# Performance work log

Measured on AMD Instinct MI355X. Metric: run time of the kernel, lower is better.

Reference implementation:

```python
import jax, jax.numpy as jnp
import numpy as np

NUM_HEADS = 16
BLOCK_SIZE = 64


def setup_inputs() -> dict:
    key = jax.random.key(0)
    ks = jax.random.split(key, 5)
    B, S, C = 2, 2047, 1024
    return {
        "x": jax.random.normal(ks[0], (B, S, C), dtype=jnp.float32),
        "global_token": jax.random.normal(ks[1], (1, 1, C), dtype=jnp.float32),
        "qkv_w": jax.random.normal(ks[2], (3 * C, C), dtype=jnp.float32) * 0.02,
        "proj_w": jax.random.normal(ks[3], (C, C), dtype=jnp.float32) * 0.02,
        "proj_b": jax.random.normal(ks[4], (C,), dtype=jnp.float32) * 0.02,
    }


def reference(x, global_token, qkv_w, proj_w, proj_b):
    B, S, C = x.shape
    H = NUM_HEADS
    D = C // H
    scale = D ** -0.5
    # prepend global token -> N = S + 1
    g = jnp.broadcast_to(global_token, (B, 1, C))
    xg = jnp.concatenate([g, x], axis=1)
    N = S + 1
    # fused qkv projection (torch Linear: x @ W^T)
    qkv = (xg @ qkv_w.T).reshape(B, N, 3, H, D)
    qkv = jnp.transpose(qkv, (2, 0, 3, 1, 4))  # [3, B, H, N, D]
    q, k, v = qkv[0], qkv[1], qkv[2]
    # block-causal mask: query t sees key j iff block(j) <= block(t)
    blk = jnp.arange(N) // BLOCK_SIZE
    mask = blk[:, None] >= blk[None, :]  # [N, N]
    attn = jnp.einsum("bhqd,bhkd->bhqk", q, k) * scale
    attn = jnp.where(mask[None, None], attn, -jnp.inf)
    attn = jax.nn.softmax(attn, axis=-1)
    out = jnp.einsum("bhqk,bhkd->bhqd", attn, v)
    out = jnp.transpose(out, (0, 2, 1, 3)).reshape(B, N, C)
    out = out[:, 1:, :]  # drop global token
    return out @ proj_w.T + proj_b
```

## Files before the change

kernel.cpp:

```cpp
#include <hip/hip_runtime.h>
#include <math.h>

typedef _Float16 h16;
typedef _Float16 half8 __attribute__((ext_vector_type(8)));
typedef float f32x4 __attribute__((ext_vector_type(4)));

#define NB 2
#define NS 2047
#define NC 1024
#define NN 2048
#define NH 16
#define ND 64

__device__ __forceinline__ void gl_lds16(const h16* g, h16* l) {
  __builtin_amdgcn_global_load_lds((const __attribute__((address_space(1))) void*)g,
                                   (__attribute__((address_space(3))) void*)l, 16, 0, 0);
}
__device__ __forceinline__ f32x4 mfma16(half8 a, half8 b, f32x4 c) {
  return __builtin_amdgcn_mfma_f32_16x16x32_f16(a, b, c, 0, 0, 0);
}

__global__ __launch_bounds__(256) void cast_xg_k(
    const float* __restrict__ x, const float* __restrict__ g, h16* __restrict__ out) {
  size_t i = ((size_t)blockIdx.x * 256 + threadIdx.x) * 16;
  const int c = (int)(i & (NC - 1));
  const int n = (int)((i >> 10) & (NN - 1));
  const int b = (int)(i >> 21);
  const float* src = (n == 0) ? (g + c) : (x + ((size_t)b * NS + (n - 1)) * NC + c);
  h16 tmp[16];
#pragma unroll
  for (int j = 0; j < 4; ++j) {
    float4 f = ((const float4*)src)[j];
    tmp[4 * j + 0] = (h16)f.x; tmp[4 * j + 1] = (h16)f.y;
    tmp[4 * j + 2] = (h16)f.z; tmp[4 * j + 3] = (h16)f.w;
  }
  *(half8*)(out + i) = *(half8*)&tmp[0];
  *(half8*)(out + i + 8) = *(half8*)&tmp[8];
}

__global__ __launch_bounds__(256) void cast_f16_k(
    const float* __restrict__ in, h16* __restrict__ out) {
  size_t i = ((size_t)blockIdx.x * 256 + threadIdx.x) * 8;
  float4 f0 = ((const float4*)(in + i))[0];
  float4 f1 = ((const float4*)(in + i))[1];
  h16 tmp[8];
  tmp[0] = (h16)f0.x; tmp[1] = (h16)f0.y; tmp[2] = (h16)f0.z; tmp[3] = (h16)f0.w;
  tmp[4] = (h16)f1.x; tmp[5] = (h16)f1.y; tmp[6] = (h16)f1.z; tmp[7] = (h16)f1.w;
  *(half8*)(out + i) = *(half8*)&tmp[0];
}

__global__ __launch_bounds__(256) void gemm_qkv_h(
    const h16* __restrict__ A, const h16* __restrict__ W, h16* __restrict__ out) {
  __shared__ h16 As[128 * 32];
  __shared__ h16 Bs[128 * 32];
  const int tid = threadIdx.x;
  const int m0 = blockIdx.y * 128, j0 = blockIdx.x * 128;
  const int wid = tid >> 6, lane = tid & 63, l15 = lane & 15, quad = lane >> 4;
  const h16* ag = A + (size_t)(m0 + wid * 32 + (lane >> 2)) * NC + (lane & 3) * 8;
  const h16* bg = W + (size_t)(j0 + wid * 32 + (lane >> 2)) * NC + (lane & 3) * 8;
  h16* lA = &As[wid * 32 * 32];
  h16* lB = &Bs[wid * 32 * 32];
  f32x4 acc[2][8];
#pragma unroll
  for (int rt = 0; rt < 2; ++rt)
#pragma unroll
    for (int ct = 0; ct < 8; ++ct) acc[rt][ct] = (f32x4){0.f, 0.f, 0.f, 0.f};

  for (int k0 = 0; k0 < NC; k0 += 32) {
    __syncthreads();
    gl_lds16(ag + k0, lA);
    gl_lds16(ag + k0 + 16 * NC, lA + 16 * 32);
    gl_lds16(bg + k0, lB);
    gl_lds16(bg + k0 + 16 * NC, lB + 16 * 32);
    __syncthreads();
    half8 af0 = *(const half8*)&As[(wid * 32 + l15) * 32 + quad * 8];
    half8 af1 = *(const half8*)&As[(wid * 32 + 16 + l15) * 32 + quad * 8];
#pragma unroll
    for (int ct = 0; ct < 8; ++ct) {
      half8 bf = *(const half8*)&Bs[(ct * 16 + l15) * 32 + quad * 8];
      acc[0][ct] = mfma16(af0, bf, acc[0][ct]);
      acc[1][ct] = mfma16(af1, bf, acc[1][ct]);
    }
  }
#pragma unroll
  for (int rt = 0; rt < 2; ++rt)
#pragma unroll
    for (int ct = 0; ct < 8; ++ct)
#pragma unroll
      for (int r = 0; r < 4; ++r) {
        const int mm = m0 + wid * 32 + rt * 16 + quad * 4 + r;
        const int jj = j0 + ct * 16 + l15;
        out[(size_t)mm * (3 * NC) + jj] = (h16)acc[rt][ct][r];
      }
}

__global__ __launch_bounds__(256) void vtrans_k(
    const h16* __restrict__ qkvh, h16* __restrict__ vT) {
  __shared__ h16 ts[64 * 72];
  const int kb = blockIdx.x, h = blockIdx.y, b = blockIdx.z;
  const int t = threadIdx.x;
  const int key = t >> 2, co = (t & 3) * 16;
  const h16* src = qkvh + (size_t)(b * NN + kb * 64 + key) * (3 * NC) + 2 * NC + h * ND + co;
  half8 v0 = *(const half8*)src;
  half8 v1 = *(const half8*)(src + 8);
  *(half8*)&ts[key * 72 + co] = v0;
  *(half8*)&ts[key * 72 + co + 8] = v1;
  __syncthreads();
  const int d = t >> 2, ko = (t & 3) * 16;
  h16 buf[16];
#pragma unroll
  for (int i = 0; i < 16; ++i) buf[i] = ts[(ko + i) * 72 + d];
  h16* dst = vT + ((size_t)(b * NH + h) * ND + d) * NN + kb * 64 + ko;
  *(half8*)dst = *(half8*)&buf[0];
  *(half8*)(dst + 8) = *(half8*)&buf[8];
}

__device__ __forceinline__ void attn_tile(
    half8 aq0, half8 aq1, const h16* Ks, const h16* Vs, h16* Pw,
    int l15, int quad, f32x4* o, float* den) {
  f32x4 s[4];
#pragma unroll
  for (int ct = 0; ct < 4; ++ct) {
    half8 bk0 = *(const half8*)&Ks[(ct * 16 + l15) * 72 + quad * 8];
    half8 bk1 = *(const half8*)&Ks[(ct * 16 + l15) * 72 + 32 + quad * 8];
    f32x4 z = (f32x4){0.f, 0.f, 0.f, 0.f};
    z = mfma16(aq0, bk0, z);
    s[ct] = mfma16(aq1, bk1, z);
  }
#pragma unroll
  for (int ct = 0; ct < 4; ++ct)
#pragma unroll
    for (int r = 0; r < 4; ++r) {
      float p = __expf(s[ct][r] * 0.125f);
      den[r] += p;
      Pw[(quad * 4 + r) * 72 + ct * 16 + l15] = (h16)p;
    }
  half8 ap0 = *(const half8*)&Pw[l15 * 72 + quad * 8];
  half8 ap1 = *(const half8*)&Pw[l15 * 72 + 32 + quad * 8];
#pragma unroll
  for (int ct = 0; ct < 4; ++ct) {
    half8 bv0 = *(const half8*)&Vs[(ct * 16 + l15) * 72 + quad * 8];
    half8 bv1 = *(const half8*)&Vs[(ct * 16 + l15) * 72 + 32 + quad * 8];
    o[ct] = mfma16(ap0, bv0, o[ct]);
    o[ct] = mfma16(ap1, bv1, o[ct]);
  }
}

__global__ __launch_bounds__(256) void attn_h(
    const h16* __restrict__ qkvh, const h16* __restrict__ vT, h16* __restrict__ outp) {
  __shared__ h16 Ks[64 * 72];
  __shared__ h16 Vs[64 * 72];
  __shared__ h16 Ps[128 * 72];
  const int q1 = blockIdx.x;
  const int q2 = 31 - q1;
  const int h = blockIdx.y, b = blockIdx.z;
  const int tid = threadIdx.x, wid = tid >> 6, lane = tid & 63;
  const int l15 = lane & 15, quad = lane >> 4;
  const h16* q1src = qkvh + (size_t)(b * NN + q1 * 64 + wid * 16 + l15) * (3 * NC) + h * ND + quad * 8;
  const h16* q2src = qkvh + (size_t)(b * NN + q2 * 64 + wid * 16 + l15) * (3 * NC) + h * ND + quad * 8;
  half8 a1q0 = *(const half8*)q1src;
  half8 a1q1 = *(const half8*)(q1src + 32);
  half8 a2q0 = *(const half8*)q2src;
  half8 a2q1 = *(const half8*)(q2src + 32);
  f32x4 o1[4], o2[4];
  float d1[4] = {0.f, 0.f, 0.f, 0.f}, d2[4] = {0.f, 0.f, 0.f, 0.f};
#pragma unroll
  for (int ct = 0; ct < 4; ++ct) {
    o1[ct] = (f32x4){0.f, 0.f, 0.f, 0.f};
    o2[ct] = (f32x4){0.f, 0.f, 0.f, 0.f};
  }
  const int skey = tid >> 2, sco = (tid & 3) * 16;
  const h16* kbase = qkvh + (size_t)(b * NN + skey) * (3 * NC) + NC + h * ND + sco;
  const h16* vbase = vT + ((size_t)(b * NH + h) * ND + skey) * NN + sco;
  h16* P1 = &Ps[(wid * 16) * 72];
  h16* P2 = &Ps[(64 + wid * 16) * 72];

  for (int kb = 0; kb <= q2; ++kb) {
    const h16* kp = kbase + (size_t)kb * 64 * (3 * NC);
    half8 k0 = *(const half8*)kp;
    half8 k1 = *(const half8*)(kp + 8);
    const h16* vp = vbase + kb * 64;
    half8 v0 = *(const half8*)vp;
    half8 v1 = *(const half8*)(vp + 8);
    __syncthreads();
    *(half8*)&Ks[skey * 72 + sco] = k0; *(half8*)&Ks[skey * 72 + sco + 8] = k1;
    *(half8*)&Vs[skey * 72 + sco] = v0; *(half8*)&Vs[skey * 72 + sco + 8] = v1;
    __syncthreads();
    attn_tile(a2q0, a2q1, Ks, Vs, P2, l15, quad, o2, d2);
    if (kb <= q1) attn_tile(a1q0, a1q1, Ks, Vs, P1, l15, quad, o1, d1);
  }
#pragma unroll
  for (int r = 0; r < 4; ++r)
#pragma unroll
    for (int off = 1; off < 16; off <<= 1) {
      d1[r] += __shfl_xor(d1[r], off);
      d2[r] += __shfl_xor(d2[r], off);
    }
#pragma unroll
  for (int ct = 0; ct < 4; ++ct)
#pragma unroll
    for (int r = 0; r < 4; ++r) {
      const int n1 = q1 * 64 + wid * 16 + quad * 4 + r;
      const int n2 = q2 * 64 + wid * 16 + quad * 4 + r;
      outp[(size_t)(b * NN + n1) * NC + h * ND + ct * 16 + l15] = (h16)(o1[ct][r] / d1[r]);
      outp[(size_t)(b * NN + n2) * NC + h * ND + ct * 16 + l15] = (h16)(o2[ct][r] / d2[r]);
    }
}

__global__ __launch_bounds__(256) void gemm_proj_h(
    const h16* __restrict__ Ah, const h16* __restrict__ W,
    const float* __restrict__ bias, float* __restrict__ out) {
  __shared__ h16 As[64 * 32];
  __shared__ h16 Bs[128 * 32];
  const int tid = threadIdx.x;
  const int m0 = blockIdx.y * 64, j0 = blockIdx.x * 128;
  const int wid = tid >> 6, lane = tid & 63, l15 = lane & 15, quad = lane >> 4;
  int m = m0 + wid * 16 + (lane >> 2);
  if (m > NB * NS - 1) m = NB * NS - 1;
  const int bb = (m >= NS) ? 1 : 0;
  const h16* ag = Ah + (size_t)(bb * NN + m - bb * NS + 1) * NC + (lane & 3) * 8;
  const h16* bg = W + (size_t)(j0 + wid * 32 + (lane >> 2)) * NC + (lane & 3) * 8;
  h16* lA = &As[wid * 16 * 32];
  h16* lB = &Bs[wid * 32 * 32];
  f32x4 acc[8];
#pragma unroll
  for (int ct = 0; ct < 8; ++ct) acc[ct] = (f32x4){0.f, 0.f, 0.f, 0.f};

  for (int k0 = 0; k0 < NC; k0 += 32) {
    __syncthreads();
    gl_lds16(ag + k0, lA);
    gl_lds16(bg + k0, lB);
    gl_lds16(bg + k0 + 16 * NC, lB + 16 * 32);
    __syncthreads();
    half8 af = *(const half8*)&As[(wid * 16 + l15) * 32 + quad * 8];
#pragma unroll
    for (int ct = 0; ct < 8; ++ct) {
      half8 bf = *(const half8*)&Bs[(ct * 16 + l15) * 32 + quad * 8];
      acc[ct] = mfma16(af, bf, acc[ct]);
    }
  }
#pragma unroll
  for (int ct = 0; ct < 8; ++ct) {
    const float bv = bias[j0 + ct * 16 + l15];
#pragma unroll
    for (int r = 0; r < 4; ++r) {
      const int mm = m0 + wid * 16 + quad * 4 + r;
      if (mm < NB * NS)
        out[(size_t)mm * NC + j0 + ct * 16 + l15] = acc[ct][r] + bv;
    }
  }
}

extern "C" void kernel_launch(void* const* d_in, const int* in_sizes, int n_in,
                              void* d_out, int out_size, void* d_ws, size_t ws_size,
                              hipStream_t stream) {
  const float* x = (const float*)d_in[0];
  const float* g = (const float*)d_in[1];
  const float* qkv_w = (const float*)d_in[2];
  const float* proj_w = (const float*)d_in[3];
  const float* proj_b = (const float*)d_in[4];
  float* out = (float*)d_out;

  h16* xgh  = (h16*)d_ws;
  h16* w3h  = xgh + (size_t)NB * NN * NC;
  h16* wph  = w3h + (size_t)3 * NC * NC;
  h16* qkvh = wph + (size_t)NC * NC;
  h16* vTh  = qkvh + (size_t)NB * NN * 3 * NC;
  h16* attnh = vTh + (size_t)NB * NH * ND * NN;

  cast_xg_k<<<dim3(1024), 256, 0, stream>>>(x, g, xgh);
  cast_f16_k<<<dim3(1536), 256, 0, stream>>>(qkv_w, w3h);
  cast_f16_k<<<dim3(512), 256, 0, stream>>>(proj_w, wph);
  gemm_qkv_h<<<dim3(24, 32), 256, 0, stream>>>(xgh, w3h, qkvh);
  vtrans_k<<<dim3(32, NH, NB), 256, 0, stream>>>(qkvh, vTh);
  attn_h<<<dim3(16, NH, NB), 256, 0, stream>>>(qkvh, vTh, attnh);
  gemm_proj_h<<<dim3(8, 64), 256, 0, stream>>>(attnh, wph, proj_b, out);
}
```

Before: 204.0 us.

## Restructure GEMMs to 2x2 warp tiles, register-stream K/V in attention, merge weight casts

Both GEMMs now use a 2x2 warp layout, load A fragments straight from global memory into registers, and stage only B in LDS in a k-major layout with a 64-wide K step. The attention kernel drops the LDS staging of K and V. Each wave loads its own K/V fragments into registers and prefetches the next K tile, uses a remapped 1D grid, and splits the loop so the short query block is handled without a per-iteration branch. The two weight-cast launches are merged into one. These changes aim to cut LDS traffic, barriers and launch count, at the cost of redundant global loads per wave and higher register pressure.

```diff
diff --git a/kernel.cpp b/kernel.cpp
--- a/kernel.cpp
+++ b/kernel.cpp
@@ -38,58 +38,71 @@
   *(half8*)(out + i + 8) = *(half8*)&tmp[8];
 }
 
-__global__ __launch_bounds__(256) void cast_f16_k(
-    const float* __restrict__ in, h16* __restrict__ out) {
+__global__ __launch_bounds__(256) void cast_w_k(
+    const float* __restrict__ qw, const float* __restrict__ pw, h16* __restrict__ out) {
   size_t i = ((size_t)blockIdx.x * 256 + threadIdx.x) * 8;
-  float4 f0 = ((const float4*)(in + i))[0];
-  float4 f1 = ((const float4*)(in + i))[1];
+  const float* src = (i < (size_t)3 * NC * NC) ? (qw + i) : (pw + (i - (size_t)3 * NC * NC));
+  float4 f0 = ((const float4*)src)[0];
+  float4 f1 = ((const float4*)src)[1];
   h16 tmp[8];
   tmp[0] = (h16)f0.x; tmp[1] = (h16)f0.y; tmp[2] = (h16)f0.z; tmp[3] = (h16)f0.w;
   tmp[4] = (h16)f1.x; tmp[5] = (h16)f1.y; tmp[6] = (h16)f1.z; tmp[7] = (h16)f1.w;
   *(half8*)(out + i) = *(half8*)&tmp[0];
 }
 
-__global__ __launch_bounds__(256) void gemm_qkv_h(
+__global__ __launch_bounds__(256, 3) void gemm_qkv_h(
     const h16* __restrict__ A, const h16* __restrict__ W, h16* __restrict__ out) {
-  __shared__ h16 As[128 * 32];
-  __shared__ h16 Bs[128 * 32];
+  __shared__ h16 Bs[8 * 128 * 8];
   const int tid = threadIdx.x;
   const int m0 = blockIdx.y * 128, j0 = blockIdx.x * 128;
   const int wid = tid >> 6, lane = tid & 63, l15 = lane & 15, quad = lane >> 4;
-  const h16* ag = A + (size_t)(m0 + wid * 32 + (lane >> 2)) * NC + (lane & 3) * 8;
-  const h16* bg = W + (size_t)(j0 + wid * 32 + (lane >> 2)) * NC + (lane & 3) * 8;
-  h16* lA = &As[wid * 32 * 32];
-  h16* lB = &Bs[wid * 32 * 32];
-  f32x4 acc[2][8];
-#pragma unroll
-  for (int rt = 0; rt < 2; ++rt)
-#pragma unroll
-    for (int ct = 0; ct < 8; ++ct) acc[rt][ct] = (f32x4){0.f, 0.f, 0.f, 0.f};
-
-  for (int k0 = 0; k0 < NC; k0 += 32) {
+  const int w0 = wid & 1, w1 = wid >> 1;
+  const h16* abase = A + (size_t)(m0 + w1 * 64 + l15) * NC + quad * 8;
+  const h16* bW = W + (size_t)(j0 + lane) * NC;
+  f32x4 acc[4][4];
+#pragma unroll
+  for (int rt = 0; rt < 4; ++rt)
+#pragma unroll
+    for (int ct = 0; ct < 4; ++ct) acc[rt][ct] = (f32x4){0.f, 0.f, 0.f, 0.f};
+
+  for (int k0 = 0; k0 < NC; k0 += 64) {
     __syncthreads();
-    gl_lds16(ag + k0, lA);
-    gl_lds16(ag + k0 + 16 * NC, lA + 16 * 32);
-    gl_lds16(bg + k0, lB);
-    gl_lds16(bg + k0 + 16 * NC, lB + 16 * 32);
+#pragma unroll
+    for (int s = 0; s < 2; ++s) {
+      const int k8 = wid * 2 + s;
+#pragma unroll
+      for (int jo = 0; jo < 2; ++jo)
+        gl_lds16(bW + (size_t)jo * 64 * NC + k0 + k8 * 8, &Bs[(k8 * 128 + jo * 64) * 8]);
+    }
     __syncthreads();
-    half8 af0 = *(const half8*)&As[(wid * 32 + l15) * 32 + quad * 8];
-    half8 af1 = *(const half8*)&As[(wid * 32 + 16 + l15) * 32 + quad * 8];
-#pragma unroll
-    for (int ct = 0; ct < 8; ++ct) {
-      half8 bf = *(const half8*)&Bs[(ct * 16 + l15) * 32 + quad * 8];
-      acc[0][ct] = mfma16(af0, bf, acc[0][ct]);
-      acc[1][ct] = mfma16(af1, bf, acc[1][ct]);
-    }
-  }
-#pragma unroll
-  for (int rt = 0; rt < 2; ++rt)
-#pragma unroll
-    for (int ct = 0; ct < 8; ++ct)
+    half8 af[4][2];
+#pragma unroll
+    for (int rt = 0; rt < 4; ++rt) {
+      af[rt][0] = *(const half8*)(abase + (size_t)rt * 16 * NC + k0);
+      af[rt][1] = *(const half8*)(abase + (size_t)rt * 16 * NC + k0 + 32);
+    }
+    half8 bf[4][2];
+#pragma unroll
+    for (int ct = 0; ct < 4; ++ct) {
+      bf[ct][0] = *(const half8*)&Bs[((quad)*128 + w0 * 64 + ct * 16 + l15) * 8];
+      bf[ct][1] = *(const half8*)&Bs[((4 + quad) * 128 + w0 * 64 + ct * 16 + l15) * 8];
+    }
+#pragma unroll
+    for (int rt = 0; rt < 4; ++rt)
+#pragma unroll
+      for (int ct = 0; ct < 4; ++ct) {
+        acc[rt][ct] = mfma16(af[rt][0], bf[ct][0], acc[rt][ct]);
+        acc[rt][ct] = mfma16(af[rt][1], bf[ct][1], acc[rt][ct]);
+      }
+  }
+#pragma unroll
+  for (int rt = 0; rt < 4; ++rt)
+#pragma unroll
+    for (int ct = 0; ct < 4; ++ct)
 #pragma unroll
       for (int r = 0; r < 4; ++r) {
-        const int mm = m0 + wid * 32 + rt * 16 + quad * 4 + r;
-        const int jj = j0 + ct * 16 + l15;
+        const int mm = m0 + w1 * 64 + rt * 16 + quad * 4 + r;
+        const int jj = j0 + w0 * 64 + ct * 16 + l15;
         out[(size_t)mm * (3 * NC) + jj] = (h16)acc[rt][ct][r];
       }
 }
@@ -115,53 +128,30 @@
   *(half8*)(dst + 8) = *(half8*)&buf[8];
 }
 
-__device__ __forceinline__ void attn_tile(
-    half8 aq0, half8 aq1, const h16* Ks, const h16* Vs, h16* Pw,
-    int l15, int quad, f32x4* o, float* den) {
-  f32x4 s[4];
-#pragma unroll
-  for (int ct = 0; ct < 4; ++ct) {
-    half8 bk0 = *(const half8*)&Ks[(ct * 16 + l15) * 72 + quad * 8];
-    half8 bk1 = *(const half8*)&Ks[(ct * 16 + l15) * 72 + 32 + quad * 8];
-    f32x4 z = (f32x4){0.f, 0.f, 0.f, 0.f};
-    z = mfma16(aq0, bk0, z);
-    s[ct] = mfma16(aq1, bk1, z);
-  }
-#pragma unroll
-  for (int ct = 0; ct < 4; ++ct)
-#pragma unroll
-    for (int r = 0; r < 4; ++r) {
-      float p = __expf(s[ct][r] * 0.125f);
-      den[r] += p;
-      Pw[(quad * 4 + r) * 72 + ct * 16 + l15] = (h16)p;
-    }
-  half8 ap0 = *(const half8*)&Pw[l15 * 72 + quad * 8];
-  half8 ap1 = *(const half8*)&Pw[l15 * 72 + 32 + quad * 8];
-#pragma unroll
-  for (int ct = 0; ct < 4; ++ct) {
-    half8 bv0 = *(const half8*)&Vs[(ct * 16 + l15) * 72 + quad * 8];
-    half8 bv1 = *(const half8*)&Vs[(ct * 16 + l15) * 72 + 32 + quad * 8];
-    o[ct] = mfma16(ap0, bv0, o[ct]);
-    o[ct] = mfma16(ap1, bv1, o[ct]);
-  }
-}
-
-__global__ __launch_bounds__(256) void attn_h(
+#define PST 68
+__global__ __launch_bounds__(256, 2) void attn_h(
     const h16* __restrict__ qkvh, const h16* __restrict__ vT, h16* __restrict__ outp) {
-  __shared__ h16 Ks[64 * 72];
-  __shared__ h16 Vs[64 * 72];
-  __shared__ h16 Ps[128 * 72];
-  const int q1 = blockIdx.x;
-  const int q2 = 31 - q1;
-  const int h = blockIdx.y, b = blockIdx.z;
+  __shared__ h16 Ps[128 * PST];
+  const int wg = blockIdx.x;
+  const int bh = (wg & 7) * 4 + ((wg >> 3) & 3);
+  const int pr = wg >> 5;
+  const int b = bh >> 4, h = bh & 15;
+  const int q1 = pr, q2 = 31 - pr;
   const int tid = threadIdx.x, wid = tid >> 6, lane = tid & 63;
   const int l15 = lane & 15, quad = lane >> 4;
+  h16* Pw2 = &Ps[(wid * 32) * PST];
+  h16* Pw1 = Pw2 + 16 * PST;
+
   const h16* q1src = qkvh + (size_t)(b * NN + q1 * 64 + wid * 16 + l15) * (3 * NC) + h * ND + quad * 8;
   const h16* q2src = qkvh + (size_t)(b * NN + q2 * 64 + wid * 16 + l15) * (3 * NC) + h * ND + quad * 8;
   half8 a1q0 = *(const half8*)q1src;
   half8 a1q1 = *(const half8*)(q1src + 32);
   half8 a2q0 = *(const half8*)q2src;
   half8 a2q1 = *(const half8*)(q2src + 32);
+
+  const h16* kp0 = qkvh + ((size_t)(b * NN + l15) * 3 + 1) * NC + h * ND + quad * 8;
+  const h16* vp0 = vT + ((size_t)(b * NH + h) * ND + l15) * NN + quad * 8;
+
   f32x4 o1[4], o2[4];
   float d1[4] = {0.f, 0.f, 0.f, 0.f}, d2[4] = {0.f, 0.f, 0.f, 0.f};
 #pragma unroll
@@ -169,26 +159,65 @@
     o1[ct] = (f32x4){0.f, 0.f, 0.f, 0.f};
     o2[ct] = (f32x4){0.f, 0.f, 0.f, 0.f};
   }
-  const int skey = tid >> 2, sco = (tid & 3) * 16;
-  const h16* kbase = qkvh + (size_t)(b * NN + skey) * (3 * NC) + NC + h * ND + sco;
-  const h16* vbase = vT + ((size_t)(b * NH + h) * ND + skey) * NN + sco;
-  h16* P1 = &Ps[(wid * 16) * 72];
-  h16* P2 = &Ps[(64 + wid * 16) * 72];
-
-  for (int kb = 0; kb <= q2; ++kb) {
-    const h16* kp = kbase + (size_t)kb * 64 * (3 * NC);
-    half8 k0 = *(const half8*)kp;
-    half8 k1 = *(const half8*)(kp + 8);
-    const h16* vp = vbase + kb * 64;
-    half8 v0 = *(const half8*)vp;
-    half8 v1 = *(const half8*)(vp + 8);
-    __syncthreads();
-    *(half8*)&Ks[skey * 72 + sco] = k0; *(half8*)&Ks[skey * 72 + sco + 8] = k1;
-    *(half8*)&Vs[skey * 72 + sco] = v0; *(half8*)&Vs[skey * 72 + sco + 8] = v1;
-    __syncthreads();
-    attn_tile(a2q0, a2q1, Ks, Vs, P2, l15, quad, o2, d2);
-    if (kb <= q1) attn_tile(a1q0, a1q1, Ks, Vs, P1, l15, quad, o1, d1);
-  }
+
+#define LOADK(kb, kf)                                                        \
+  {                                                                          \
+    const h16* p_ = kp0 + (size_t)(kb) * 64 * (3 * NC);                      \
+    _Pragma("unroll") for (int ct = 0; ct < 4; ++ct) {                       \
+      kf[2 * ct] = *(const half8*)(p_ + (size_t)ct * 16 * (3 * NC));         \
+      kf[2 * ct + 1] = *(const half8*)(p_ + (size_t)ct * 16 * (3 * NC) + 32);\
+    }                                                                        \
+  }
+#define LOADV(kb, vf)                                                        \
+  {                                                                          \
+    const h16* p_ = vp0 + (kb) * 64;                                         \
+    _Pragma("unroll") for (int ct = 0; ct < 4; ++ct) {                       \
+      vf[2 * ct] = *(const half8*)(p_ + (size_t)ct * 16 * NN);               \
+      vf[2 * ct + 1] = *(const half8*)(p_ + (size_t)ct * 16 * NN + 32);      \
+    }                                                                        \
+  }
+#define TILE(aq0, aq1, kf, vf, Pw, o, den)                                   \
+  {                                                                          \
+    f32x4 s_[4];                                                             \
+    _Pragma("unroll") for (int ct = 0; ct < 4; ++ct) {                       \
+      f32x4 z_ = (f32x4){0.f, 0.f, 0.f, 0.f};                                \
+      z_ = mfma16(aq0, kf[2 * ct], z_);                                      \
+      s_[ct] = mfma16(aq1, kf[2 * ct + 1], z_);                              \
+    }                                                                        \
+    _Pragma("unroll") for (int ct = 0; ct < 4; ++ct)                         \
+        _Pragma("unroll") for (int r = 0; r < 4; ++r) {                      \
+      float p_ = __expf(s_[ct][r] * 0.125f);                                 \
+      den[r] += p_;                                                          \
+      Pw[(quad * 4 + r) * PST + ct * 16 + l15] = (h16)p_;                    \
+    }                                                                        \
+    half8 ap0_ = *(const half8*)&Pw[l15 * PST + quad * 8];                   \
+    half8 ap1_ = *(const half8*)&Pw[l15 * PST + 32 + quad * 8];              \
+    _Pragma("unroll") for (int ct = 0; ct < 4; ++ct) {                       \
+      o[ct] = mfma16(ap0_, vf[2 * ct], o[ct]);                               \
+      o[ct] = mfma16(ap1_, vf[2 * ct + 1], o[ct]);                           \
+    }                                                                        \
+  }
+
+  half8 kf[8], kfn[8], vf[8];
+  LOADK(0, kf);
+  for (int kb = 0; kb <= q1; ++kb) {
+    LOADV(kb, vf);
+    const int nkb = (kb + 1 <= q2) ? kb + 1 : q2;
+    LOADK(nkb, kfn);
+    TILE(a2q0, a2q1, kf, vf, Pw2, o2, d2);
+    TILE(a1q0, a1q1, kf, vf, Pw1, o1, d1);
+#pragma unroll
+    for (int i = 0; i < 8; ++i) kf[i] = kfn[i];
+  }
+  for (int kb = q1 + 1; kb <= q2; ++kb) {
+    LOADV(kb, vf);
+    const int nkb = (kb + 1 <= q2) ? kb + 1 : q2;
+    LOADK(nkb, kfn);
+    TILE(a2q0, a2q1, kf, vf, Pw2, o2, d2);
+#pragma unroll
+    for (int i = 0; i < 8; ++i) kf[i] = kfn[i];
+  }
+
 #pragma unroll
   for (int r = 0; r < 4; ++r)
 #pragma unroll
@@ -207,48 +236,71 @@
     }
 }
 
-__global__ __launch_bounds__(256) void gemm_proj_h(
+__global__ __launch_bounds__(256, 2) void gemm_proj_h(
     const h16* __restrict__ Ah, const h16* __restrict__ W,
     const float* __restrict__ bias, float* __restrict__ out) {
-  __shared__ h16 As[64 * 32];
-  __shared__ h16 Bs[128 * 32];
+  __shared__ h16 Bs[8 * 128 * 8];
   const int tid = threadIdx.x;
   const int m0 = blockIdx.y * 64, j0 = blockIdx.x * 128;
   const int wid = tid >> 6, lane = tid & 63, l15 = lane & 15, quad = lane >> 4;
-  int m = m0 + wid * 16 + (lane >> 2);
-  if (m > NB * NS - 1) m = NB * NS - 1;
-  const int bb = (m >= NS) ? 1 : 0;
-  const h16* ag = Ah + (size_t)(bb * NN + m - bb * NS + 1) * NC + (lane & 3) * 8;
-  const h16* bg = W + (size_t)(j0 + wid * 32 + (lane >> 2)) * NC + (lane & 3) * 8;
-  h16* lA = &As[wid * 16 * 32];
-  h16* lB = &Bs[wid * 32 * 32];
-  f32x4 acc[8];
-#pragma unroll
-  for (int ct = 0; ct < 8; ++ct) acc[ct] = (f32x4){0.f, 0.f, 0.f, 0.f};
-
-  for (int k0 = 0; k0 < NC; k0 += 32) {
+  const int w0 = wid & 1, w1 = wid >> 1;
+  const h16* abase[2];
+#pragma unroll
+  for (int rt = 0; rt < 2; ++rt) {
+    int m = m0 + w1 * 32 + rt * 16 + l15;
+    if (m > NB * NS - 1) m = NB * NS - 1;
+    const int bb = (m >= NS) ? 1 : 0;
+    abase[rt] = Ah + (size_t)(bb * NN + m - bb * NS + 1) * NC + quad * 8;
+  }
+  const h16* bW = W + (size_t)(j0 + lane) * NC;
+  f32x4 acc[2][4];
+#pragma unroll
+  for (int rt = 0; rt < 2; ++rt)
+#pragma unroll
+    for (int ct = 0; ct < 4; ++ct) acc[rt][ct] = (f32x4){0.f, 0.f, 0.f, 0.f};
+
+  for (int k0 = 0; k0 < NC; k0 += 64) {
     __syncthreads();
-    gl_lds16(ag + k0, lA);
-    gl_lds16(bg + k0, lB);
-    gl_lds16(bg + k0 + 16 * NC, lB + 16 * 32);
+#pragma unroll
+    for (int s = 0; s < 2; ++s) {
+      const int k8 = wid * 2 + s;
+#pragma unroll
+      for (int jo = 0; jo < 2; ++jo)
+        gl_lds16(bW + (size_t)jo * 64 * NC + k0 + k8 * 8, &Bs[(k8 * 128 + jo * 64) * 8]);
+    }
     __syncthreads();
-    half8 af = *(const half8*)&As[(wid * 16 + l15) * 32 + quad * 8];
-#pragma unroll
-    for (int ct = 0; ct < 8; ++ct) {
-      half8 bf = *(const half8*)&Bs[(ct * 16 + l15) * 32 + quad * 8];
-      acc[ct] = mfma16(af, bf, acc[ct]);
-    }
-  }
-#pragma unroll
-  for (int ct = 0; ct < 8; ++ct) {
-    const float bv = bias[j0 + ct * 16 + l15];
-#pragma unroll
-    for (int r = 0; r < 4; ++r) {
-      const int mm = m0 + wid * 16 + quad * 4 + r;
-      if (mm < NB * NS)
-        out[(size_t)mm * NC + j0 + ct * 16 + l15] = acc[ct][r] + bv;
-    }
-  }
+    half8 af[2][2];
+#pragma unroll
+    for (int rt = 0; rt < 2; ++rt) {
+      af[rt][0] = *(const half8*)(abase[rt] + k0);
+      af[rt][1] = *(const half8*)(abase[rt] + k0 + 32);
+    }
+    half8 bf[4][2];
+#pragma unroll
+    for (int ct = 0; ct < 4; ++ct) {
+      bf[ct][0] = *(const half8*)&Bs[((quad)*128 + w0 * 64 + ct * 16 + l15) * 8];
+      bf[ct][1] = *(const half8*)&Bs[((4 + quad) * 128 + w0 * 64 + ct * 16 + l15) * 8];
+    }
+#pragma unroll
+    for (int rt = 0; rt < 2; ++rt)
+#pragma unroll
+      for (int ct = 0; ct < 4; ++ct) {
+        acc[rt][ct] = mfma16(af[rt][0], bf[ct][0], acc[rt][ct]);
+        acc[rt][ct] = mfma16(af[rt][1], bf[ct][1], acc[rt][ct]);
+      }
+  }
+#pragma unroll
+  for (int rt = 0; rt < 2; ++rt)
+#pragma unroll
+    for (int ct = 0; ct < 4; ++ct) {
+      const int jj = j0 + w0 * 64 + ct * 16 + l15;
+      const float bv = bias[jj];
+#pragma unroll
+      for (int r = 0; r < 4; ++r) {
+        const int mm = m0 + w1 * 32 + rt * 16 + quad * 4 + r;
+        if (mm < NB * NS) out[(size_t)mm * NC + jj] = acc[rt][ct][r] + bv;
+      }
+    }
 }
 
 extern "C" void kernel_launch(void* const* d_in, const int* in_sizes, int n_in,
@@ -269,10 +321,9 @@
   h16* attnh = vTh + (size_t)NB * NH * ND * NN;
 
   cast_xg_k<<<dim3(1024), 256, 0, stream>>>(x, g, xgh);
-  cast_f16_k<<<dim3(1536), 256, 0, stream>>>(qkv_w, w3h);
-  cast_f16_k<<<dim3(512), 256, 0, stream>>>(proj_w, wph);
+  cast_w_k<<<dim3(2048), 256, 0, stream>>>(qkv_w, proj_w, w3h);
   gemm_qkv_h<<<dim3(24, 32), 256, 0, stream>>>(xgh, w3h, qkvh);
   vtrans_k<<<dim3(32, NH, NB), 256, 0, stream>>>(qkvh, vTh);
-  attn_h<<<dim3(16, NH, NB), 256, 0, stream>>>(qkvh, vTh, attnh);
+  attn_h<<<dim3(512), 256, 0, stream>>>(qkvh, vTh, attnh);
   gemm_proj_h<<<dim3(8, 64), 256, 0, stream>>>(attnh, wph, proj_b, out);
 }
```

After: 299.5 us. 46.8% more time.

## Rewrite attention with per-wave key split and double-buffered async loads; widen GEMM K-tiles

Applied to the files above, without the earlier changes.

Attention now launches one block per query tile, ordered longest first. Each of the four waves handles a disjoint quarter of every key block, loaded asynchronously into double-buffered LDS with waitcnt-based per-wave sync, and the partial outputs and denominators are reduced across waves through LDS at the end. P is kept in registers by feeding it to a 16x16x16 MFMA as the B operand, which removes the LDS round trip for P. Both GEMMs move to 64-wide K tiles with XOR-swizzled LDS, and the two weight casts merge into one launch. This targets LDS traffic, the per-iteration block barriers and launch overhead, at the cost of more LDS use and an extra cross-wave reduction.

```diff
diff --git a/kernel.cpp b/kernel.cpp
--- a/kernel.cpp
+++ b/kernel.cpp
@@ -3,6 +3,7 @@
 
 typedef _Float16 h16;
 typedef _Float16 half8 __attribute__((ext_vector_type(8)));
+typedef _Float16 half4 __attribute__((ext_vector_type(4)));
 typedef float f32x4 __attribute__((ext_vector_type(4)));
 
 #define NB 2
@@ -16,9 +17,14 @@
   __builtin_amdgcn_global_load_lds((const __attribute__((address_space(1))) void*)g,
                                    (__attribute__((address_space(3))) void*)l, 16, 0, 0);
 }
-__device__ __forceinline__ f32x4 mfma16(half8 a, half8 b, f32x4 c) {
+__device__ __forceinline__ f32x4 mfma32(half8 a, half8 b, f32x4 c) {
   return __builtin_amdgcn_mfma_f32_16x16x32_f16(a, b, c, 0, 0, 0);
 }
+__device__ __forceinline__ f32x4 mfma16x(half4 a, half4 b, f32x4 c) {
+  return __builtin_amdgcn_mfma_f32_16x16x16f16(a, b, c, 0, 0, 0);
+}
+#define WAITVM4 __builtin_amdgcn_s_waitcnt(0x0F74)
+#define WAITLG0 __builtin_amdgcn_s_waitcnt(0xC07F)
 
 __global__ __launch_bounds__(256) void cast_xg_k(
     const float* __restrict__ x, const float* __restrict__ g, h16* __restrict__ out) {
@@ -38,11 +44,12 @@
   *(half8*)(out + i + 8) = *(half8*)&tmp[8];
 }
 
-__global__ __launch_bounds__(256) void cast_f16_k(
-    const float* __restrict__ in, h16* __restrict__ out) {
+__global__ __launch_bounds__(256) void cast_w_k(
+    const float* __restrict__ qw, const float* __restrict__ pw, h16* __restrict__ out) {
   size_t i = ((size_t)blockIdx.x * 256 + threadIdx.x) * 8;
-  float4 f0 = ((const float4*)(in + i))[0];
-  float4 f1 = ((const float4*)(in + i))[1];
+  const float* src = (i < (size_t)3 * NC * NC) ? (qw + i) : (pw + (i - (size_t)3 * NC * NC));
+  float4 f0 = ((const float4*)src)[0];
+  float4 f1 = ((const float4*)src)[1];
   h16 tmp[8];
   tmp[0] = (h16)f0.x; tmp[1] = (h16)f0.y; tmp[2] = (h16)f0.z; tmp[3] = (h16)f0.w;
   tmp[4] = (h16)f1.x; tmp[5] = (h16)f1.y; tmp[6] = (h16)f1.z; tmp[7] = (h16)f1.w;
@@ -51,35 +58,39 @@
 
 __global__ __launch_bounds__(256) void gemm_qkv_h(
     const h16* __restrict__ A, const h16* __restrict__ W, h16* __restrict__ out) {
-  __shared__ h16 As[128 * 32];
-  __shared__ h16 Bs[128 * 32];
+  __shared__ h16 As[128 * 64];
+  __shared__ h16 Bs[128 * 64];
   const int tid = threadIdx.x;
   const int m0 = blockIdx.y * 128, j0 = blockIdx.x * 128;
   const int wid = tid >> 6, lane = tid & 63, l15 = lane & 15, quad = lane >> 4;
-  const h16* ag = A + (size_t)(m0 + wid * 32 + (lane >> 2)) * NC + (lane & 3) * 8;
-  const h16* bg = W + (size_t)(j0 + wid * 32 + (lane >> 2)) * NC + (lane & 3) * 8;
-  h16* lA = &As[wid * 32 * 32];
-  h16* lB = &Bs[wid * 32 * 32];
+  const int rl = lane >> 3, cp = lane & 7, csw = cp ^ rl;
+  const h16* ag = A + (size_t)(m0 + wid * 32 + rl) * NC + csw * 8;
+  const h16* bg = W + (size_t)(j0 + wid * 32 + rl) * NC + csw * 8;
   f32x4 acc[2][8];
 #pragma unroll
   for (int rt = 0; rt < 2; ++rt)
 #pragma unroll
     for (int ct = 0; ct < 8; ++ct) acc[rt][ct] = (f32x4){0.f, 0.f, 0.f, 0.f};
 
-  for (int k0 = 0; k0 < NC; k0 += 32) {
-    __syncthreads();
-    gl_lds16(ag + k0, lA);
-    gl_lds16(ag + k0 + 16 * NC, lA + 16 * 32);
-    gl_lds16(bg + k0, lB);
-    gl_lds16(bg + k0 + 16 * NC, lB + 16 * 32);
-    __syncthreads();
-    half8 af0 = *(const half8*)&As[(wid * 32 + l15) * 32 + quad * 8];
-    half8 af1 = *(const half8*)&As[(wid * 32 + 16 + l15) * 32 + quad * 8];
-#pragma unroll
-    for (int ct = 0; ct < 8; ++ct) {
-      half8 bf = *(const half8*)&Bs[(ct * 16 + l15) * 32 + quad * 8];
-      acc[0][ct] = mfma16(af0, bf, acc[0][ct]);
-      acc[1][ct] = mfma16(af1, bf, acc[1][ct]);
+  for (int k0 = 0; k0 < NC; k0 += 64) {
+    __syncthreads();
+#pragma unroll
+    for (int i = 0; i < 4; ++i) {
+      gl_lds16(ag + (size_t)i * 8 * NC + k0, &As[(wid * 32 + i * 8) * 64]);
+      gl_lds16(bg + (size_t)i * 8 * NC + k0, &Bs[(wid * 32 + i * 8) * 64]);
+    }
+    __syncthreads();
+#pragma unroll
+    for (int ks = 0; ks < 2; ++ks) {
+      const int p0 = ((ks * 4 + quad) ^ (l15 & 7)) * 8;
+      half8 af0 = *(const half8*)&As[(wid * 32 + l15) * 64 + p0];
+      half8 af1 = *(const half8*)&As[(wid * 32 + 16 + l15) * 64 + p0];
+#pragma unroll
+      for (int ct = 0; ct < 8; ++ct) {
+        half8 bf = *(const half8*)&Bs[(ct * 16 + l15) * 64 + p0];
+        acc[0][ct] = mfma32(af0, bf, acc[0][ct]);
+        acc[1][ct] = mfma32(af1, bf, acc[1][ct]);
+      }
     }
   }
 #pragma unroll
@@ -115,128 +126,201 @@
   *(half8*)(dst + 8) = *(half8*)&buf[8];
 }
 
-__device__ __forceinline__ void attn_tile(
-    half8 aq0, half8 aq1, const h16* Ks, const h16* Vs, h16* Pw,
-    int l15, int quad, f32x4* o, float* den) {
-  f32x4 s[4];
-#pragma unroll
-  for (int ct = 0; ct < 4; ++ct) {
-    half8 bk0 = *(const half8*)&Ks[(ct * 16 + l15) * 72 + quad * 8];
-    half8 bk1 = *(const half8*)&Ks[(ct * 16 + l15) * 72 + 32 + quad * 8];
-    f32x4 z = (f32x4){0.f, 0.f, 0.f, 0.f};
-    z = mfma16(aq0, bk0, z);
-    s[ct] = mfma16(aq1, bk1, z);
-  }
-#pragma unroll
-  for (int ct = 0; ct < 4; ++ct)
-#pragma unroll
-    for (int r = 0; r < 4; ++r) {
-      float p = __expf(s[ct][r] * 0.125f);
-      den[r] += p;
-      Pw[(quad * 4 + r) * 72 + ct * 16 + l15] = (h16)p;
-    }
-  half8 ap0 = *(const half8*)&Pw[l15 * 72 + quad * 8];
-  half8 ap1 = *(const half8*)&Pw[l15 * 72 + 32 + quad * 8];
-#pragma unroll
-  for (int ct = 0; ct < 4; ++ct) {
-    half8 bv0 = *(const half8*)&Vs[(ct * 16 + l15) * 72 + quad * 8];
-    half8 bv1 = *(const half8*)&Vs[(ct * 16 + l15) * 72 + 32 + quad * 8];
-    o[ct] = mfma16(ap0, bv0, o[ct]);
-    o[ct] = mfma16(ap1, bv1, o[ct]);
-  }
-}
-
-__global__ __launch_bounds__(256) void attn_h(
+__global__ __launch_bounds__(256, 3) void attn_h(
     const h16* __restrict__ qkvh, const h16* __restrict__ vT, h16* __restrict__ outp) {
-  __shared__ h16 Ks[64 * 72];
-  __shared__ h16 Vs[64 * 72];
-  __shared__ h16 Ps[128 * 72];
-  const int q1 = blockIdx.x;
-  const int q2 = 31 - q1;
-  const int h = blockIdx.y, b = blockIdx.z;
-  const int tid = threadIdx.x, wid = tid >> 6, lane = tid & 63;
+  __shared__ h16 K0[4][1024];
+  __shared__ h16 V0[4][1024];
+  __shared__ h16 K1[4][1024];
+  __shared__ h16 V1[4][1024];
+  __shared__ float RED[2 * 64 * 36];
+  __shared__ float DEN[4 * 64];
+  const int bx = blockIdx.x;
+  const int qb = 31 - (bx >> 5);
+  const int bh = bx & 31;
+  const int b = bh >> 4, h = bh & 15;
+  const int tid = threadIdx.x, w = tid >> 6, lane = tid & 63;
   const int l15 = lane & 15, quad = lane >> 4;
-  const h16* q1src = qkvh + (size_t)(b * NN + q1 * 64 + wid * 16 + l15) * (3 * NC) + h * ND + quad * 8;
-  const h16* q2src = qkvh + (size_t)(b * NN + q2 * 64 + wid * 16 + l15) * (3 * NC) + h * ND + quad * 8;
-  half8 a1q0 = *(const half8*)q1src;
-  half8 a1q1 = *(const half8*)(q1src + 32);
-  half8 a2q0 = *(const half8*)q2src;
-  half8 a2q1 = *(const half8*)(q2src + 32);
-  f32x4 o1[4], o2[4];
-  float d1[4] = {0.f, 0.f, 0.f, 0.f}, d2[4] = {0.f, 0.f, 0.f, 0.f};
-#pragma unroll
-  for (int ct = 0; ct < 4; ++ct) {
-    o1[ct] = (f32x4){0.f, 0.f, 0.f, 0.f};
-    o2[ct] = (f32x4){0.f, 0.f, 0.f, 0.f};
-  }
-  const int skey = tid >> 2, sco = (tid & 3) * 16;
-  const h16* kbase = qkvh + (size_t)(b * NN + skey) * (3 * NC) + NC + h * ND + sco;
-  const h16* vbase = vT + ((size_t)(b * NH + h) * ND + skey) * NN + sco;
-  h16* P1 = &Ps[(wid * 16) * 72];
-  h16* P2 = &Ps[(64 + wid * 16) * 72];
-
-  for (int kb = 0; kb <= q2; ++kb) {
-    const h16* kp = kbase + (size_t)kb * 64 * (3 * NC);
-    half8 k0 = *(const half8*)kp;
-    half8 k1 = *(const half8*)(kp + 8);
-    const h16* vp = vbase + kb * 64;
-    half8 v0 = *(const half8*)vp;
-    half8 v1 = *(const half8*)(vp + 8);
-    __syncthreads();
-    *(half8*)&Ks[skey * 72 + sco] = k0; *(half8*)&Ks[skey * 72 + sco + 8] = k1;
-    *(half8*)&Vs[skey * 72 + sco] = v0; *(half8*)&Vs[skey * 72 + sco + 8] = v1;
-    __syncthreads();
-    attn_tile(a2q0, a2q1, Ks, Vs, P2, l15, quad, o2, d2);
-    if (kb <= q1) attn_tile(a1q0, a1q1, Ks, Vs, P1, l15, quad, o1, d1);
-  }
-#pragma unroll
-  for (int r = 0; r < 4; ++r)
-#pragma unroll
-    for (int off = 1; off < 16; off <<= 1) {
-      d1[r] += __shfl_xor(d1[r], off);
-      d2[r] += __shfl_xor(d2[r], off);
-    }
-#pragma unroll
-  for (int ct = 0; ct < 4; ++ct)
-#pragma unroll
-    for (int r = 0; r < 4; ++r) {
-      const int n1 = q1 * 64 + wid * 16 + quad * 4 + r;
-      const int n2 = q2 * 64 + wid * 16 + quad * 4 + r;
-      outp[(size_t)(b * NN + n1) * NC + h * ND + ct * 16 + l15] = (h16)(o1[ct][r] / d1[r]);
-      outp[(size_t)(b * NN + n2) * NC + h * ND + ct * 16 + l15] = (h16)(o2[ct][r] / d2[r]);
-    }
+
+  half8 bq[4][2];
+#pragma unroll
+  for (int nt = 0; nt < 4; ++nt) {
+    const h16* qp = qkvh + (size_t)(b * NN + qb * 64 + nt * 16 + l15) * (3 * NC) + h * ND + quad * 8;
+    half8 t0 = *(const half8*)qp;
+    half8 t1 = *(const half8*)(qp + 32);
+    bq[nt][0] = t0 * (h16)0.125f;
+    bq[nt][1] = t1 * (h16)0.125f;
+  }
+
+  const int rl = lane >> 3, csw = (lane & 7) ^ rl;
+  const h16* ksrc = qkvh + ((size_t)(b * NN + w * 16 + rl) * 3 + 1) * NC + h * ND + csw * 8;
+  const h16* vsrc = vT + ((size_t)(b * NH + h) * ND + (lane >> 1)) * NN + w * 16 + (lane & 1) * 8;
+
+  const int ka0 = l15 * 64 + ((quad) ^ (l15 & 7)) * 8;
+  const int ka1 = l15 * 64 + ((quad + 4) ^ (l15 & 7)) * 8;
+
+  f32x4 o[4][4];
+  float den[4] = {0.f, 0.f, 0.f, 0.f};
+#pragma unroll
+  for (int mt = 0; mt < 4; ++mt)
+#pragma unroll
+    for (int nt = 0; nt < 4; ++nt) o[mt][nt] = (f32x4){0.f, 0.f, 0.f, 0.f};
+
+#define STAGE(Kd, Vd, kb)                                 \
+  {                                                       \
+    const h16* kp_ = ksrc + (size_t)(kb) * (64 * 3 * NC); \
+    const h16* vp_ = vsrc + (kb) * 64;                    \
+    gl_lds16(kp_, &Kd[w][0]);                             \
+    gl_lds16(kp_ + (size_t)8 * 3 * NC, &Kd[w][512]);      \
+    gl_lds16(vp_, &Vd[w][0]);                             \
+    gl_lds16(vp_ + (size_t)32 * NN, &Vd[w][512]);         \
+  }
+
+#define COMPUTE(Kd, Vd)                                                       \
+  {                                                                           \
+    half8 kf0 = *(const half8*)&Kd[w][ka0];                                   \
+    half8 kf1 = *(const half8*)&Kd[w][ka1];                                   \
+    half4 vf[4];                                                              \
+    _Pragma("unroll") for (int mt = 0; mt < 4; ++mt)                          \
+        vf[mt] = *(const half4*)&Vd[w][(mt * 16 + l15) * 16 + quad * 4];      \
+    _Pragma("unroll") for (int nt = 0; nt < 4; ++nt) {                        \
+      f32x4 s = (f32x4){0.f, 0.f, 0.f, 0.f};                                  \
+      s = mfma32(kf0, bq[nt][0], s);                                          \
+      s = mfma32(kf1, bq[nt][1], s);                                          \
+      float e0 = __expf(s[0]), e1 = __expf(s[1]);                             \
+      float e2 = __expf(s[2]), e3 = __expf(s[3]);                             \
+      den[nt] += (e0 + e1) + (e2 + e3);                                       \
+      int2 pi;                                                                \
+      pi.x = __builtin_bit_cast(int, __builtin_amdgcn_cvt_pkrtz(e0, e1));     \
+      pi.y = __builtin_bit_cast(int, __builtin_amdgcn_cvt_pkrtz(e2, e3));     \
+      half4 p = __builtin_bit_cast(half4, pi);                                \
+      _Pragma("unroll") for (int mt = 0; mt < 4; ++mt)                        \
+          o[mt][nt] = mfma16x(vf[mt], p, o[mt][nt]);                          \
+    }                                                                         \
+  }
+
+  STAGE(K0, V0, 0);
+  {
+    const int k1 = (qb >= 1) ? 1 : 0;
+    STAGE(K1, V1, k1);
+  }
+  for (int kb = 0; kb <= qb; kb += 2) {
+    WAITVM4;
+    __builtin_amdgcn_wave_barrier();
+    COMPUTE(K0, V0);
+    WAITLG0;
+    __builtin_amdgcn_wave_barrier();
+    {
+      const int nk = (kb + 2 <= qb) ? kb + 2 : kb;
+      STAGE(K0, V0, nk);
+    }
+    if (kb + 1 <= qb) {
+      WAITVM4;
+      __builtin_amdgcn_wave_barrier();
+      COMPUTE(K1, V1);
+      WAITLG0;
+      __builtin_amdgcn_wave_barrier();
+      {
+        const int nk = (kb + 3 <= qb) ? kb + 3 : kb + 1;
+        STAGE(K1, V1, nk);
+      }
+    }
+  }
+
+#pragma unroll
+  for (int nt = 0; nt < 4; ++nt) {
+    den[nt] += __shfl_xor(den[nt], 16);
+    den[nt] += __shfl_xor(den[nt], 32);
+  }
+  __syncthreads();
+  if (quad == 0) {
+#pragma unroll
+    for (int nt = 0; nt < 4; ++nt) DEN[w * 64 + nt * 16 + l15] = den[nt];
+  }
+#pragma unroll
+  for (int r = 0; r < 2; ++r) {
+    if (r) __syncthreads();
+    if (w < 2) {
+#pragma unroll
+      for (int mt2 = 0; mt2 < 2; ++mt2)
+#pragma unroll
+        for (int nt = 0; nt < 4; ++nt)
+          *(f32x4*)&RED[(w * 64 + nt * 16 + l15) * 36 + mt2 * 16 + quad * 4] =
+              o[r * 2 + mt2][nt];
+    }
+    __syncthreads();
+    if (w >= 2) {
+#pragma unroll
+      for (int mt2 = 0; mt2 < 2; ++mt2)
+#pragma unroll
+        for (int nt = 0; nt < 4; ++nt) {
+          float* p = &RED[((w - 2) * 64 + nt * 16 + l15) * 36 + mt2 * 16 + quad * 4];
+          f32x4 t = *(f32x4*)p;
+          *(f32x4*)p = t + o[r * 2 + mt2][nt];
+        }
+    }
+    __syncthreads();
+    {
+      const int q = w * 16 + l15;
+      const float dt = DEN[q] + DEN[64 + q] + DEN[128 + q] + DEN[192 + q];
+      const float inv = 1.f / dt;
+      f32x4 x0 = *(const f32x4*)&RED[(0 * 64 + q) * 36 + quad * 8];
+      f32x4 x1 = *(const f32x4*)&RED[(0 * 64 + q) * 36 + quad * 8 + 4];
+      f32x4 y0 = *(const f32x4*)&RED[(1 * 64 + q) * 36 + quad * 8];
+      f32x4 y1 = *(const f32x4*)&RED[(1 * 64 + q) * 36 + quad * 8 + 4];
+      x0 += y0;
+      x1 += y1;
+      int4 pk;
+      pk.x = __builtin_bit_cast(int, __builtin_amdgcn_cvt_pkrtz(x0[0] * inv, x0[1] * inv));
+      pk.y = __builtin_bit_cast(int, __builtin_amdgcn_cvt_pkrtz(x0[2] * inv, x0[3] * inv));
+      pk.z = __builtin_bit_cast(int, __builtin_amdgcn_cvt_pkrtz(x1[0] * inv, x1[1] * inv));
+      pk.w = __builtin_bit_cast(int, __builtin_amdgcn_cvt_pkrtz(x1[2] * inv, x1[3] * inv));
+      h16* op = outp + (size_t)(b * NN + qb * 64 + q) * NC + h * ND + r * 32 + quad * 8;
+      *(half8*)op = __builtin_bit_cast(half8, pk);
+    }
+  }
+#undef STAGE
+#undef COMPUTE
 }
 
 __global__ __launch_bounds__(256) void gemm_proj_h(
     const h16* __restrict__ Ah, const h16* __restrict__ W,
     const float* __restrict__ bias, float* __restrict__ out) {
-  __shared__ h16 As[64 * 32];
-  __shared__ h16 Bs[128 * 32];
+  __shared__ h16 As[64 * 64];
+  __shared__ h16 Bs[128 * 64];
   const int tid = threadIdx.x;
   const int m0 = blockIdx.y * 64, j0 = blockIdx.x * 128;
   const int wid = tid >> 6, lane = tid & 63, l15 = lane & 15, quad = lane >> 4;
-  int m = m0 + wid * 16 + (lane >> 2);
-  if (m > NB * NS - 1) m = NB * NS - 1;
-  const int bb = (m >= NS) ? 1 : 0;
-  const h16* ag = Ah + (size_t)(bb * NN + m - bb * NS + 1) * NC + (lane & 3) * 8;
-  const h16* bg = W + (size_t)(j0 + wid * 32 + (lane >> 2)) * NC + (lane & 3) * 8;
-  h16* lA = &As[wid * 16 * 32];
-  h16* lB = &Bs[wid * 32 * 32];
+  const int rl = lane >> 3, csw = (lane & 7) ^ rl;
+  const h16* ag[2];
+#pragma unroll
+  for (int i = 0; i < 2; ++i) {
+    int m = m0 + wid * 16 + i * 8 + rl;
+    if (m > NB * NS - 1) m = NB * NS - 1;
+    const int bb = (m >= NS) ? 1 : 0;
+    ag[i] = Ah + (size_t)(bb * NN + m - bb * NS + 1) * NC + csw * 8;
+  }
+  const h16* bg = W + (size_t)(j0 + wid * 32 + rl) * NC + csw * 8;
   f32x4 acc[8];
 #pragma unroll
   for (int ct = 0; ct < 8; ++ct) acc[ct] = (f32x4){0.f, 0.f, 0.f, 0.f};
 
-  for (int k0 = 0; k0 < NC; k0 += 32) {
-    __syncthreads();
-    gl_lds16(ag + k0, lA);
-    gl_lds16(bg + k0, lB);
-    gl_lds16(bg + k0 + 16 * NC, lB + 16 * 32);
-    __syncthreads();
-    half8 af = *(const half8*)&As[(wid * 16 + l15) * 32 + quad * 8];
-#pragma unroll
-    for (int ct = 0; ct < 8; ++ct) {
-      half8 bf = *(const half8*)&Bs[(ct * 16 + l15) * 32 + quad * 8];
-      acc[ct] = mfma16(af, bf, acc[ct]);
+  for (int k0 = 0; k0 < NC; k0 += 64) {
+    __syncthreads();
+    gl_lds16(ag[0] + k0, &As[(wid * 16) * 64]);
+    gl_lds16(ag[1] + k0, &As[(wid * 16 + 8) * 64]);
+#pragma unroll
+    for (int i = 0; i < 4; ++i)
+      gl_lds16(bg + (size_t)i * 8 * NC + k0, &Bs[(wid * 32 + i * 8) * 64]);
+    __syncthreads();
+#pragma unroll
+    for (int ks = 0; ks < 2; ++ks) {
+      const int p0 = ((ks * 4 + quad) ^ (l15 & 7)) * 8;
+      half8 af = *(const half8*)&As[(wid * 16 + l15) * 64 + p0];
+#pragma unroll
+      for (int ct = 0; ct < 8; ++ct) {
+        half8 bf = *(const half8*)&Bs[(ct * 16 + l15) * 64 + p0];
+        acc[ct] = mfma32(af, bf, acc[ct]);
+      }
     }
   }
 #pragma unroll
@@ -269,10 +353,9 @@
   h16* attnh = vTh + (size_t)NB * NH * ND * NN;
 
   cast_xg_k<<<dim3(1024), 256, 0, stream>>>(x, g, xgh);
-  cast_f16_k<<<dim3(1536), 256, 0, stream>>>(qkv_w, w3h);
-  cast_f16_k<<<dim3(512), 256, 0, stream>>>(proj_w, wph);
+  cast_w_k<<<dim3(2048), 256, 0, stream>>>(qkv_w, proj_w, w3h);
   gemm_qkv_h<<<dim3(24, 32), 256, 0, stream>>>(xgh, w3h, qkvh);
   vtrans_k<<<dim3(32, NH, NB), 256, 0, stream>>>(qkvh, vTh);
-  attn_h<<<dim3(16, NH, NB), 256, 0, stream>>>(qkvh, vTh, attnh);
+  attn_h<<<dim3(1024), 256, 0, stream>>>(qkvh, vTh, attnh);
   gemm_proj_h<<<dim3(8, 64), 256, 0, stream>>>(attnh, wph, proj_b, out);
 }
```

Measured after the change: 183.2 us. -10.2%, faster.
